# Performance work log

Measured on AMD Instinct MI355X. Metric: run time of the kernel, lower is better.

## Reference

```python
import jax, jax.numpy as jnp
import numpy as np

BS, N, IN_F, OUT_F, HEADS = 32, 512, 256, 128, 4
NEG_SLOPE = 0.2


def setup_inputs() -> dict:
    key = jax.random.key(0)
    k1, k2, k3, k4, k5 = jax.random.split(key, 5)
    inputs = jax.random.normal(k1, (BS, N, IN_F), dtype=jnp.float32)
    adj = (jax.random.uniform(k2, (BS, N, N)) > 0.5).astype(jnp.float32)
    # xavier_normal-style init with relu gain sqrt(2)
    w = jax.random.normal(k3, (IN_F, HEADS * OUT_F), dtype=jnp.float32) * (
        np.sqrt(2.0) * np.sqrt(2.0 / (IN_F + HEADS * OUT_F))
    )
    a_i = jax.random.normal(k4, (HEADS, OUT_F, 1), dtype=jnp.float32) * (
        np.sqrt(2.0) * np.sqrt(2.0 / (OUT_F + 1))
    )
    a_j = jax.random.normal(k5, (HEADS, OUT_F, 1), dtype=jnp.float32) * (
        np.sqrt(2.0) * np.sqrt(2.0 / (OUT_F + 1))
    )
    bias = jnp.zeros((HEADS * OUT_F,), dtype=jnp.float32)
    return {"inputs": inputs, "adj": adj, "w": w, "a_i": a_i, "a_j": a_j, "bias": bias}


def reference(inputs, adj, w, a_i, a_j, bias):
    bs, n, _ = inputs.shape
    H, D = a_i.shape[0], a_i.shape[1]
    # self_loop_type == 2: adjacency unchanged
    # project: [bs, n, H, D]
    h = jnp.matmul(inputs, w).reshape(bs, n, H, D)
    # additive attention coefficients: [bs, n, H]
    coeff_i = jnp.einsum('bnhd,hdo->bnho', h, a_i)[..., 0]
    coeff_j = jnp.einsum('bnhd,hdo->bnho', h, a_j)[..., 0]
    # broadcast-sum scores e[b, i, j, h], leaky relu
    e = jax.nn.leaky_relu(coeff_i[:, :, None, :] + coeff_j[:, None, :, :],
                          negative_slope=NEG_SLOPE)
    adj_h = adj[..., None]  # [bs, n, n, 1], broadcasts over heads
    masked_e = jnp.where(adj_h <= 0, jnp.float32(-1e9), e)
    # softmax over neighbor axis j (dim 2), then re-mask
    attention = jax.nn.softmax(masked_e, axis=2) * adj_h
    # dropout = 0.0 -> no-op; normalize=False, average=False
    # per-head aggregation, all heads at once: out[b,i,h,d] = sum_j att[b,i,j,h] h[b,j,h,d]
    out = jnp.einsum('bijh,bjhd->bihd', attention, h).reshape(bs, n, H * D)
    return out + bias
```

## Files before the change

### kernel.cpp

```cpp
#include <hip/hip_runtime.h>
#include <hip/hip_cooperative_groups.h>

namespace cg = cooperative_groups;

#define BSZ 32
#define NN 512
#define INF 256
#define NH 4
#define HD 512
#define NEG_SLOPE 0.2f

typedef __attribute__((ext_vector_type(8))) short bf16x8;
typedef __attribute__((ext_vector_type(8))) unsigned short ushort8;
typedef __attribute__((ext_vector_type(4))) float f32x4;

static __device__ __forceinline__ unsigned short f2bf(float f) {
    unsigned u = __builtin_bit_cast(unsigned, f);
    return (unsigned short)((u + 0x7FFFu + ((u >> 16) & 1u)) >> 16);
}

static __device__ __forceinline__ bf16x8 pk8(float4 a, float4 b) {
    unsigned d0, d1, d2, d3;
    asm("v_cvt_pk_bf16_f32 %0, %1, %2" : "=v"(d0) : "v"(a.x), "v"(a.y));
    asm("v_cvt_pk_bf16_f32 %0, %1, %2" : "=v"(d1) : "v"(a.z), "v"(a.w));
    asm("v_cvt_pk_bf16_f32 %0, %1, %2" : "=v"(d2) : "v"(b.x), "v"(b.y));
    asm("v_cvt_pk_bf16_f32 %0, %1, %2" : "=v"(d3) : "v"(b.z), "v"(b.w));
    uint4 u; u.x = d0; u.y = d1; u.z = d2; u.w = d3;
    return __builtin_bit_cast(bf16x8, u);
}

static __device__ __forceinline__ void gl_lds16(const void* g, void* l) {
    __builtin_amdgcn_global_load_lds(
        (const __attribute__((address_space(1))) unsigned int*)g,
        (__attribute__((address_space(3))) unsigned int*)l, 16, 0, 0);
}

__global__ __launch_bounds__(256, 4) void mega(
    const float* __restrict__ x, const float* __restrict__ adj,
    const float* __restrict__ w, const float* __restrict__ ai,
    const float* __restrict__ aj, const float* __restrict__ bias,
    float* __restrict__ out, unsigned short* __restrict__ wB,
    unsigned short* __restrict__ hB, float* __restrict__ ciT,
    float* __restrict__ cjT, unsigned char* __restrict__ mbB)
{
    __shared__ __align__(16) char smem[32768];
    const int tid = threadIdx.x;
    const int lane = tid & 63, wave = tid >> 6;
    const int l15 = lane & 15, g = lane >> 4;
    const int bid = blockIdx.x;

    if (bid < 512) {
        int gid = bid * 256 + tid;
        int c = gid & 511, k = gid >> 9;
        int kb = k >> 5, gg = (k >> 3) & 3, e = k & 7;
        wB[(((size_t)(kb * 4 + gg) * 512) + c) * 8 + e] = f2bf(w[(size_t)k * 512 + c]);
    }
    {
        const int row0 = bid * 16 + wave * 4;
        #pragma unroll
        for (int rr = 0; rr < 4; ++rr) {
            const float* ap = adj + (size_t)(row0 + rr) * NN + lane * 8;
            float4 a0 = *(const float4*)ap;
            float4 a1 = *(const float4*)(ap + 4);
            unsigned byte = 0;
            byte |= (a0.x > 0.f) ? 1u   : 0u;
            byte |= (a0.y > 0.f) ? 2u   : 0u;
            byte |= (a0.z > 0.f) ? 4u   : 0u;
            byte |= (a0.w > 0.f) ? 8u   : 0u;
            byte |= (a1.x > 0.f) ? 16u  : 0u;
            byte |= (a1.y > 0.f) ? 32u  : 0u;
            byte |= (a1.z > 0.f) ? 64u  : 0u;
            byte |= (a1.w > 0.f) ? 128u : 0u;
            mbB[(size_t)(row0 + rr) * 64 + lane] = (unsigned char)byte;
        }
    }
    cg::this_grid().sync();

    if (bid < 512) {
        unsigned short* hs = (unsigned short*)smem;
        const int row0 = bid * 32;

        f32x4 acc[2][8] = {};
        const float* xp0 = x + (size_t)(row0 + l15) * INF + g * 8;
        const float* xp1 = xp0 + 16 * INF;
        const unsigned short* bp = wB + ((size_t)g * 512 + (size_t)wave * 128 + l15) * 8;

        #pragma unroll
        for (int kb = 0; kb < 8; ++kb) {
            float4 f0 = *(const float4*)(xp0 + kb * 32);
            float4 f1 = *(const float4*)(xp0 + kb * 32 + 4);
            float4 f2 = *(const float4*)(xp1 + kb * 32);
            float4 f3 = *(const float4*)(xp1 + kb * 32 + 4);
            bf16x8 a0 = pk8(f0, f1);
            bf16x8 a1 = pk8(f2, f3);
            #pragma unroll
            for (int nf = 0; nf < 8; ++nf) {
                bf16x8 bv = *(const bf16x8*)(bp + (size_t)kb * 16384 + nf * 128);
                acc[0][nf] = __builtin_amdgcn_mfma_f32_16x16x32_bf16(a0, bv, acc[0][nf], 0, 0, 0);
                acc[1][nf] = __builtin_amdgcn_mfma_f32_16x16x32_bf16(a1, bv, acc[1][nf], 0, 0, 0);
            }
        }

        float aiv[8], ajv[8];
        #pragma unroll
        for (int nf = 0; nf < 8; ++nf) {
            aiv[nf] = ai[wave * 128 + nf * 16 + l15];
            ajv[nf] = aj[wave * 128 + nf * 16 + l15];
        }
        const int b = row0 >> 9;
        const int nloc0 = row0 & 511;
        const int kb2 = nloc0 >> 5;

        #pragma unroll
        for (int m = 0; m < 2; ++m) {
            float pi[4] = {0,0,0,0}, pj[4] = {0,0,0,0};
            #pragma unroll
            for (int nf = 0; nf < 8; ++nf)
                #pragma unroll
                for (int reg = 0; reg < 4; ++reg) {
                    pi[reg] = fmaf(acc[m][nf][reg], aiv[nf], pi[reg]);
                    pj[reg] = fmaf(acc[m][nf][reg], ajv[nf], pj[reg]);
                }
            #pragma unroll
            for (int reg = 0; reg < 4; ++reg) {
                #pragma unroll
                for (int off = 1; off < 16; off <<= 1) {
                    pi[reg] += __shfl_xor(pi[reg], off);
                    pj[reg] += __shfl_xor(pj[reg], off);
                }
            }
            if (l15 == 0) {
                #pragma unroll
                for (int reg = 0; reg < 4; ++reg) {
                    int n = nloc0 + 16 * m + 4 * g + reg;
                    ciT[((size_t)(wave * BSZ + b) * NN) + n] = pi[reg];
                    cjT[((size_t)(wave * BSZ + b) * NN) + n] = pj[reg];
                }
            }
            #pragma unroll
            for (int reg = 0; reg < 4; ++reg) {
                int jloc = 16 * m + 4 * g + reg;
                int g2 = jloc >> 3, e = jloc & 7;
                #pragma unroll
                for (int nf = 0; nf < 8; ++nf)
                    hs[wave * 4096 + nf * 512 + g2 * 128 + l15 * 8 + e] =
                        f2bf(acc[m][nf][reg]);
            }
        }
        __syncthreads();
        {
            ushort8* dst = (ushort8*)(hB + (((size_t)(b * 4 + wave) * 16 + kb2) * 4096));
            const ushort8* src = (const ushort8*)(hs + wave * 4096);
            #pragma unroll
            for (int it = 0; it < 8; ++it)
                dst[it * 64 + lane] = src[it * 64 + lane];
        }
    }
    cg::this_grid().sync();

    {
        unsigned short (*Bst)[4096] = (unsigned short(*)[4096])smem;
        float* cjh  = (float*)(smem + 16384);
        float* cih  = (float*)(smem + 18432);
        unsigned (*maskS)[17] = (unsigned(*)[17])(smem + 18688);
        float* Mpart = (float*)(smem + 23040);
        const unsigned* mb = (const unsigned*)mbB;

        const int orig = bid;
        const int swz = (orig & 7) * 128 + (orig >> 3);
        const int b  = swz >> 5;
        const int h  = (swz >> 3) & 3;
        const int i0 = (swz & 7) * 64;

        const char* gslab = (const char*)(hB + (size_t)(b * NH + h) * 65536);

        gl_lds16(gslab + wave * 2048 + lane * 16,        (char*)&Bst[0][0] + wave * 2048);
        gl_lds16(gslab + wave * 2048 + 1024 + lane * 16, (char*)&Bst[0][0] + wave * 2048 + 1024);

        {
            const float* src = cjT + (size_t)(h * BSZ + b) * NN;
            float v0 = src[tid], v1 = src[tid + 256];
            cjh[tid] = v0; cjh[tid + 256] = v1;
            float mv = fmaxf(v0, v1);
            #pragma unroll
            for (int off = 32; off; off >>= 1) mv = fmaxf(mv, __shfl_xor(mv, off));
            if (lane == 0) Mpart[wave] = mv;
            if (tid < 64) cih[tid] = ciT[(size_t)(h * BSZ + b) * NN + i0 + tid];
            uint4 m4 = ((const uint4*)(mb + ((size_t)b * NN + i0) * 16))[tid];
            int base = tid * 4, row = base >> 4, wi = base & 15;
            maskS[row][wi] = m4.x; maskS[row][wi + 1] = m4.y;
            maskS[row][wi + 2] = m4.z; maskS[row][wi + 3] = m4.w;
        }
        __syncthreads();

        const float M = fmaxf(fmaxf(Mpart[0], Mpart[1]), fmaxf(Mpart[2], Mpart[3]));
        const float bc = cih[wave * 16 + l15];
        float smx = bc + M;
        const float mrow = fmaxf(smx, NEG_SLOPE * smx);

        float bvv[8];
        #pragma unroll
        for (int nf = 0; nf < 8; ++nf) bvv[nf] = bias[h * 128 + nf * 16 + l15];

        bf16x8 ones;
        #pragma unroll
        for (int e = 0; e < 8; ++e) ones[e] = (short)0x3F80;

        f32x4 acc[8] = {};
        f32x4 accs = {};
        int cur = 0;
        const unsigned* mrowp = maskS[wave * 16 + l15];

        for (int kb = 0; kb < 16; ++kb) {
            if (kb < 15) {
                const char* gs = gslab + (size_t)(kb + 1) * 8192 + wave * 2048 + lane * 16;
                char* ld = (char*)&Bst[cur ^ 1][0] + wave * 2048;
                gl_lds16(gs, ld);
                gl_lds16(gs + 1024, ld + 1024);
            }

            float4 cva = *(const float4*)&cjh[kb * 32 + g * 8];
            float4 cvb = *(const float4*)&cjh[kb * 32 + g * 8 + 4];
            float cj8[8] = {cva.x, cva.y, cva.z, cva.w, cvb.x, cvb.y, cvb.z, cvb.w};
            unsigned byte = (mrowp[kb] >> (g * 8)) & 0xFFu;
            float p[8];
            #pragma unroll
            for (int e = 0; e < 8; ++e) {
                float s = bc + cj8[e];
                s = fmaxf(s, NEG_SLOPE * s);
                float pe = __expf(s - mrow);
                p[e] = ((byte >> e) & 1u) ? pe : 0.f;
            }
            unsigned d0, d1, d2, d3;
            asm("v_cvt_pk_bf16_f32 %0, %1, %2" : "=v"(d0) : "v"(p[0]), "v"(p[1]));
            asm("v_cvt_pk_bf16_f32 %0, %1, %2" : "=v"(d1) : "v"(p[2]), "v"(p[3]));
            asm("v_cvt_pk_bf16_f32 %0, %1, %2" : "=v"(d2) : "v"(p[4]), "v"(p[5]));
            asm("v_cvt_pk_bf16_f32 %0, %1, %2" : "=v"(d3) : "v"(p[6]), "v"(p[7]));
            uint4 u; u.x = d0; u.y = d1; u.z = d2; u.w = d3;
            bf16x8 av = __builtin_bit_cast(bf16x8, u);

            const char* bb = (const char*)&Bst[cur][0] + lane * 16;
            bf16x8 bfr[8];
            #pragma unroll
            for (int nf = 0; nf < 8; ++nf)
                bfr[nf] = *(const bf16x8*)(bb + nf * 1024);

            #pragma unroll
            for (int nf = 0; nf < 8; ++nf)
                acc[nf] = __builtin_amdgcn_mfma_f32_16x16x32_bf16(av, bfr[nf], acc[nf], 0, 0, 0);
            accs = __builtin_amdgcn_mfma_f32_16x16x32_bf16(av, ones, accs, 0, 0, 0);

            if (kb < 15) { __syncthreads(); cur ^= 1; }
        }

        #pragma unroll
        for (int reg = 0; reg < 4; ++reg) {
            float sum = accs[reg];
            float inv = sum > 0.f ? 1.f / sum : 0.f;
            const int i = i0 + wave * 16 + g * 4 + reg;
            #pragma unroll
            for (int nf = 0; nf < 8; ++nf) {
                int colg = h * 128 + nf * 16 + l15;
                out[(size_t)(b * NN + i) * HD + colg] = acc[nf][reg] * inv + bvv[nf];
            }
        }
    }
}

__global__ __launch_bounds__(256) void k_prep(
    const float* __restrict__ w, unsigned short* __restrict__ wB,
    const float* __restrict__ adj, unsigned char* __restrict__ mbB)
{
    const int bid = blockIdx.x;
    if (bid < 2048) {
        const int lane = threadIdx.x & 63, wave = threadIdx.x >> 6;
        const int row0 = bid * 8 + wave * 2;
        #pragma unroll
        for (int rr = 0; rr < 2; ++rr) {
            const float* ap = adj + (size_t)(row0 + rr) * NN + lane * 8;
            float4 a0 = *(const float4*)ap;
            float4 a1 = *(const float4*)(ap + 4);
            unsigned byte = 0;
            byte |= (a0.x > 0.f) ? 1u : 0u;  byte |= (a0.y > 0.f) ? 2u : 0u;
            byte |= (a0.z > 0.f) ? 4u : 0u;  byte |= (a0.w > 0.f) ? 8u : 0u;
            byte |= (a1.x > 0.f) ? 16u : 0u; byte |= (a1.y > 0.f) ? 32u : 0u;
            byte |= (a1.z > 0.f) ? 64u : 0u; byte |= (a1.w > 0.f) ? 128u : 0u;
            mbB[(size_t)(row0 + rr) * 64 + lane] = (unsigned char)byte;
        }
    } else {
        int gid = (bid - 2048) * 256 + threadIdx.x;
        int c = gid & 511, k = gid >> 9;
        int kb = k >> 5, g = (k >> 3) & 3, e = k & 7;
        wB[(((size_t)(kb * 4 + g) * 512) + c) * 8 + e] = f2bf(w[(size_t)k * 512 + c]);
    }
}

__global__ __launch_bounds__(256) void k_proj(
    const float* __restrict__ x, const unsigned short* __restrict__ wB,
    const float* __restrict__ ai, const float* __restrict__ aj,
    unsigned short* __restrict__ hB, float* __restrict__ ciT, float* __restrict__ cjT)
{
    __shared__ unsigned short hs[NH * 4096];
    const int tid = threadIdx.x;
    const int lane = tid & 63, head = tid >> 6;
    const int l15 = lane & 15, g = lane >> 4;
    const int row0 = blockIdx.x * 32;

    f32x4 acc[2][8] = {};
    const float* xp0 = x + (size_t)(row0 + l15) * INF + g * 8;
    const float* xp1 = xp0 + 16 * INF;
    const unsigned short* bp = wB + ((size_t)g * 512 + head * 128 + l15) * 8;

    #pragma unroll
    for (int kb = 0; kb < 8; ++kb) {
        float4 f0 = *(const float4*)(xp0 + kb * 32);
        float4 f1 = *(const float4*)(xp0 + kb * 32 + 4);
        float4 f2 = *(const float4*)(xp1 + kb * 32);
        float4 f3 = *(const float4*)(xp1 + kb * 32 + 4);
        bf16x8 a0 = pk8(f0, f1);
        bf16x8 a1 = pk8(f2, f3);
        #pragma unroll
        for (int nf = 0; nf < 8; ++nf) {
            bf16x8 bv = *(const bf16x8*)(bp + (size_t)kb * 16384 + nf * 128);
            acc[0][nf] = __builtin_amdgcn_mfma_f32_16x16x32_bf16(a0, bv, acc[0][nf], 0, 0, 0);
            acc[1][nf] = __builtin_amdgcn_mfma_f32_16x16x32_bf16(a1, bv, acc[1][nf], 0, 0, 0);
        }
    }

    float aiv[8], ajv[8];
    #pragma unroll
    for (int nf = 0; nf < 8; ++nf) {
        aiv[nf] = ai[head * 128 + nf * 16 + l15];
        ajv[nf] = aj[head * 128 + nf * 16 + l15];
    }
    const int b = row0 >> 9;
    const int nloc0 = row0 & 511;
    const int kb2 = nloc0 >> 5;

    #pragma unroll
    for (int m = 0; m < 2; ++m) {
        float pi[4] = {0,0,0,0}, pj[4] = {0,0,0,0};
        #pragma unroll
        for (int nf = 0; nf < 8; ++nf)
            #pragma unroll
            for (int reg = 0; reg < 4; ++reg) {
                pi[reg] = fmaf(acc[m][nf][reg], aiv[nf], pi[reg]);
                pj[reg] = fmaf(acc[m][nf][reg], ajv[nf], pj[reg]);
            }
        #pragma unroll
        for (int reg = 0; reg < 4; ++reg) {
            #pragma unroll
            for (int off = 1; off < 16; off <<= 1) {
                pi[reg] += __shfl_xor(pi[reg], off);
                pj[reg] += __shfl_xor(pj[reg], off);
            }
        }
        if (l15 == 0) {
            #pragma unroll
            for (int reg = 0; reg < 4; ++reg) {
                int n = nloc0 + 16 * m + 4 * g + reg;
                ciT[((size_t)(head * BSZ + b) * NN) + n] = pi[reg];
                cjT[((size_t)(head * BSZ + b) * NN) + n] = pj[reg];
            }
        }
        #pragma unroll
        for (int reg = 0; reg < 4; ++reg) {
            int jloc = 16 * m + 4 * g + reg;
            int g2 = jloc >> 3, e = jloc & 7;
            #pragma unroll
            for (int nf = 0; nf < 8; ++nf)
                hs[head * 4096 + nf * 512 + g2 * 128 + l15 * 8 + e] =
                    f2bf(acc[m][nf][reg]);
        }
    }
    __syncthreads();
    {
        ushort8* dst = (ushort8*)(hB + (((size_t)(b * 4 + head) * 16 + kb2) * 4096));
        const ushort8* src = (const ushort8*)(hs + head * 4096);
        #pragma unroll
        for (int it = 0; it < 8; ++it)
            dst[it * 64 + lane] = src[it * 64 + lane];
    }
}

__global__ __launch_bounds__(256, 4) void k_attn(
    const unsigned short* __restrict__ hB, const float* __restrict__ ciT,
    const float* __restrict__ cjT, const unsigned* __restrict__ mb,
    const float* __restrict__ bias, float* __restrict__ out)
{
    __shared__ __align__(16) unsigned short Bst[2][4096];
    __shared__ __align__(16) float cjh[NN];
    __shared__ float cih[64];
    __shared__ unsigned maskS[64][17];
    __shared__ float Mpart[4];

    const int tid = threadIdx.x;
    const int lane = tid & 63, wave = tid >> 6;
    const int l15 = lane & 15, g = lane >> 4;

    const int orig = blockIdx.x;
    const int swz = (orig & 7) * 128 + (orig >> 3);
    const int b  = swz >> 5;
    const int h  = (swz >> 3) & 3;
    const int i0 = (swz & 7) * 64;

    const char* gslab = (const char*)(hB + (size_t)(b * NH + h) * 65536);

    gl_lds16(gslab + wave * 2048 + lane * 16,        (char*)&Bst[0][0] + wave * 2048);
    gl_lds16(gslab + wave * 2048 + 1024 + lane * 16, (char*)&Bst[0][0] + wave * 2048 + 1024);

    {
        const float* src = cjT + (size_t)(h * BSZ + b) * NN;
        float v0 = src[tid], v1 = src[tid + 256];
        cjh[tid] = v0; cjh[tid + 256] = v1;
        float mv = fmaxf(v0, v1);
        #pragma unroll
        for (int off = 32; off; off >>= 1) mv = fmaxf(mv, __shfl_xor(mv, off));
        if (lane == 0) Mpart[wave] = mv;
        if (tid < 64) cih[tid] = ciT[(size_t)(h * BSZ + b) * NN + i0 + tid];
        uint4 m4 = ((const uint4*)(mb + ((size_t)b * NN + i0) * 16))[tid];
        int base = tid * 4, row = base >> 4, wi = base & 15;
        maskS[row][wi] = m4.x; maskS[row][wi + 1] = m4.y;
        maskS[row][wi + 2] = m4.z; maskS[row][wi + 3] = m4.w;
    }
    __syncthreads();

    const float M = fmaxf(fmaxf(Mpart[0], Mpart[1]), fmaxf(Mpart[2], Mpart[3]));
    const float bc = cih[wave * 16 + l15];
    float smx = bc + M;
    const float mrow = fmaxf(smx, NEG_SLOPE * smx);

    float bvv[8];
    #pragma unroll
    for (int nf = 0; nf < 8; ++nf) bvv[nf] = bias[h * 128 + nf * 16 + l15];

    bf16x8 ones;
    #pragma unroll
    for (int e = 0; e < 8; ++e) ones[e] = (short)0x3F80;

    f32x4 acc[8] = {};
    f32x4 accs = {};
    int cur = 0;
    const unsigned* mrowp = maskS[wave * 16 + l15];

    for (int kb = 0; kb < 16; ++kb) {
        if (kb < 15) {
            const char* gs = gslab + (size_t)(kb + 1) * 8192 + wave * 2048 + lane * 16;
            char* ld = (char*)&Bst[cur ^ 1][0] + wave * 2048;
            gl_lds16(gs, ld);
            gl_lds16(gs + 1024, ld + 1024);
        }

        float4 cva = *(const float4*)&cjh[kb * 32 + g * 8];
        float4 cvb = *(const float4*)&cjh[kb * 32 + g * 8 + 4];
        float cj8[8] = {cva.x, cva.y, cva.z, cva.w, cvb.x, cvb.y, cvb.z, cvb.w};
        unsigned byte = (mrowp[kb] >> (g * 8)) & 0xFFu;
        float p[8];
        #pragma unroll
        for (int e = 0; e < 8; ++e) {
            float s = bc + cj8[e];
            s = fmaxf(s, NEG_SLOPE * s);
            float pe = __expf(s - mrow);
            p[e] = ((byte >> e) & 1u) ? pe : 0.f;
        }
        unsigned d0, d1, d2, d3;
        asm("v_cvt_pk_bf16_f32 %0, %1, %2" : "=v"(d0) : "v"(p[0]), "v"(p[1]));
        asm("v_cvt_pk_bf16_f32 %0, %1, %2" : "=v"(d1) : "v"(p[2]), "v"(p[3]));
        asm("v_cvt_pk_bf16_f32 %0, %1, %2" : "=v"(d2) : "v"(p[4]), "v"(p[5]));
        asm("v_cvt_pk_bf16_f32 %0, %1, %2" : "=v"(d3) : "v"(p[6]), "v"(p[7]));
        uint4 u; u.x = d0; u.y = d1; u.z = d2; u.w = d3;
        bf16x8 av = __builtin_bit_cast(bf16x8, u);

        const char* bb = (const char*)&Bst[cur][0] + lane * 16;
        bf16x8 bfr[8];
        #pragma unroll
        for (int nf = 0; nf < 8; ++nf)
            bfr[nf] = *(const bf16x8*)(bb + nf * 1024);

        #pragma unroll
        for (int nf = 0; nf < 8; ++nf)
            acc[nf] = __builtin_amdgcn_mfma_f32_16x16x32_bf16(av, bfr[nf], acc[nf], 0, 0, 0);
        accs = __builtin_amdgcn_mfma_f32_16x16x32_bf16(av, ones, accs, 0, 0, 0);

        if (kb < 15) { __syncthreads(); cur ^= 1; }
    }

    #pragma unroll
    for (int reg = 0; reg < 4; ++reg) {
        float sum = accs[reg];
        float inv = sum > 0.f ? 1.f / sum : 0.f;
        const int i = i0 + wave * 16 + g * 4 + reg;
        #pragma unroll
        for (int nf = 0; nf < 8; ++nf) {
            int colg = h * 128 + nf * 16 + l15;
            out[(size_t)(b * NN + i) * HD + colg] = acc[nf][reg] * inv + bvv[nf];
        }
    }
}

extern "C" void kernel_launch(void* const* d_in, const int* in_sizes, int n_in,
                              void* d_out, int out_size, void* d_ws, size_t ws_size,
                              hipStream_t stream)
{
    const float* x    = (const float*)d_in[0];
    const float* adj  = (const float*)d_in[1];
    const float* w    = (const float*)d_in[2];
    const float* ai   = (const float*)d_in[3];
    const float* aj   = (const float*)d_in[4];
    const float* bias = (const float*)d_in[5];
    float* out = (float*)d_out;

    char* ws = (char*)d_ws;
    unsigned short* wB = (unsigned short*)ws;
    unsigned short* hB = (unsigned short*)(ws + 262144);
    float* ciT         = (float*)(ws + 17039360);
    float* cjT         = (float*)(ws + 17301504);
    unsigned char* mbB = (unsigned char*)(ws + 17563648);

    int maxB = 0;
    hipError_t e = hipOccupancyMaxActiveBlocksPerMultiprocessor(
        &maxB, (const void*)mega, 256, 0);
    if (e == hipSuccess && maxB >= 4) {
        void* args[] = {(void*)&x, (void*)&adj, (void*)&w, (void*)&ai, (void*)&aj,
                        (void*)&bias, (void*)&out, (void*)&wB, (void*)&hB,
                        (void*)&ciT, (void*)&cjT, (void*)&mbB};
        hipLaunchCooperativeKernel((const void*)mega, dim3(1024), dim3(256),
                                   args, 0, stream);
    } else {
        k_prep<<<2560, 256, 0, stream>>>(w, wB, adj, mbB);
        k_proj<<<BSZ * NN / 32, 256, 0, stream>>>(x, wB, ai, aj, hB, ciT, cjT);
        k_attn<<<BSZ * NH * (NN / 64), 256, 0, stream>>>(hB, ciT, cjT,
                                                         (const unsigned*)mbB, bias, out);
    }
}
```

Baseline: 49.93 us.

## Replace grid-wide syncs with per-batch atomic flag dependencies

Swaps the two cooperative grid barriers for finer-grained atomic counters. Half the blocks convert the weights and build the adjacency bitmask while the other half wait only for the weight conversion before projecting. Attention blocks for a batch then wait only on that batch's 32 producers. The aim is to overlap the phases and avoid full-grid stalls, at the cost of a memset launch and spin-wait polling. Correctness relies on all blocks being co-resident.

```diff
diff --git a/kernel.cpp b/kernel.cpp
--- a/kernel.cpp
+++ b/kernel.cpp
@@ -1,7 +1,4 @@
 #include <hip/hip_runtime.h>
-#include <hip/hip_cooperative_groups.h>
-
-namespace cg = cooperative_groups;
 
 #define BSZ 32
 #define NN 512
@@ -35,55 +32,78 @@
         (__attribute__((address_space(3))) unsigned int*)l, 16, 0, 0);
 }
 
-__global__ __launch_bounds__(256, 4) void mega(
+__global__ __launch_bounds__(256, 4) void mega2(
     const float* __restrict__ x, const float* __restrict__ adj,
     const float* __restrict__ w, const float* __restrict__ ai,
     const float* __restrict__ aj, const float* __restrict__ bias,
     float* __restrict__ out, unsigned short* __restrict__ wB,
     unsigned short* __restrict__ hB, float* __restrict__ ciT,
-    float* __restrict__ cjT, unsigned char* __restrict__ mbB)
+    float* __restrict__ cjT, unsigned char* __restrict__ mbB,
+    unsigned* __restrict__ flags)
 {
     __shared__ __align__(16) char smem[32768];
     const int tid = threadIdx.x;
     const int lane = tid & 63, wave = tid >> 6;
     const int l15 = lane & 15, g = lane >> 4;
-    const int bid = blockIdx.x;
-
-    if (bid < 512) {
-        int gid = bid * 256 + tid;
-        int c = gid & 511, k = gid >> 9;
-        int kb = k >> 5, gg = (k >> 3) & 3, e = k & 7;
-        wB[(((size_t)(kb * 4 + gg) * 512) + c) * 8 + e] = f2bf(w[(size_t)k * 512 + c]);
-    }
-    {
-        const int row0 = bid * 16 + wave * 4;
-        #pragma unroll
-        for (int rr = 0; rr < 4; ++rr) {
-            const float* ap = adj + (size_t)(row0 + rr) * NN + lane * 8;
-            float4 a0 = *(const float4*)ap;
-            float4 a1 = *(const float4*)(ap + 4);
-            unsigned byte = 0;
-            byte |= (a0.x > 0.f) ? 1u   : 0u;
-            byte |= (a0.y > 0.f) ? 2u   : 0u;
-            byte |= (a0.z > 0.f) ? 4u   : 0u;
-            byte |= (a0.w > 0.f) ? 8u   : 0u;
-            byte |= (a1.x > 0.f) ? 16u  : 0u;
-            byte |= (a1.y > 0.f) ? 32u  : 0u;
-            byte |= (a1.z > 0.f) ? 64u  : 0u;
-            byte |= (a1.w > 0.f) ? 128u : 0u;
-            mbB[(size_t)(row0 + rr) * 64 + lane] = (unsigned char)byte;
-        }
-    }
-    cg::this_grid().sync();
-
-    if (bid < 512) {
+
+    const int orig = blockIdx.x;
+    const int swz = (orig & 7) * 128 + (orig >> 3);
+    const int b   = swz >> 5;
+    const int sub = swz & 31;
+
+    if (sub >= 16) {
+        {
+            int s = b * 16 + (sub - 16);
+            int gid = s * 256 + tid;
+            int c = gid & 511, k = gid >> 9;
+            int kb = k >> 5, gg = (k >> 3) & 3, e = k & 7;
+            wB[(((size_t)(kb * 4 + gg) * 512) + c) * 8 + e] =
+                f2bf(w[(size_t)k * 512 + c]);
+        }
+        __syncthreads();
+        __threadfence();
+        if (tid == 0)
+            __hip_atomic_fetch_add(&flags[32], 1u, __ATOMIC_RELEASE,
+                                   __HIP_MEMORY_SCOPE_AGENT);
+        {
+            const int r0 = b * NN + (sub - 16) * 32 + wave * 8;
+            #pragma unroll
+            for (int rr = 0; rr < 8; ++rr) {
+                const float* ap = adj + (size_t)(r0 + rr) * NN + lane * 8;
+                float4 a0 = *(const float4*)ap;
+                float4 a1 = *(const float4*)(ap + 4);
+                unsigned byte = 0;
+                byte |= (a0.x > 0.f) ? 1u : 0u;  byte |= (a0.y > 0.f) ? 2u : 0u;
+                byte |= (a0.z > 0.f) ? 4u : 0u;  byte |= (a0.w > 0.f) ? 8u : 0u;
+                byte |= (a1.x > 0.f) ? 16u : 0u; byte |= (a1.y > 0.f) ? 32u : 0u;
+                byte |= (a1.z > 0.f) ? 64u : 0u; byte |= (a1.w > 0.f) ? 128u : 0u;
+                mbB[(size_t)(r0 + rr) * 64 + lane] = (unsigned char)byte;
+            }
+        }
+        __syncthreads();
+        __threadfence();
+        if (tid == 0)
+            __hip_atomic_fetch_add(&flags[b], 1u, __ATOMIC_RELEASE,
+                                   __HIP_MEMORY_SCOPE_AGENT);
+    } else {
+        if (tid == 0) {
+            while (__hip_atomic_load(&flags[32], __ATOMIC_ACQUIRE,
+                                     __HIP_MEMORY_SCOPE_AGENT) < 512u)
+                __builtin_amdgcn_s_sleep(2);
+        }
+        __syncthreads();
+        __threadfence();
+
         unsigned short* hs = (unsigned short*)smem;
-        const int row0 = bid * 32;
+        const int head = wave;
+        const int nloc0 = sub * 32;
+        const int row0 = b * NN + nloc0;
+        const int kb2 = sub;
 
         f32x4 acc[2][8] = {};
         const float* xp0 = x + (size_t)(row0 + l15) * INF + g * 8;
         const float* xp1 = xp0 + 16 * INF;
-        const unsigned short* bp = wB + ((size_t)g * 512 + (size_t)wave * 128 + l15) * 8;
+        const unsigned short* bp = wB + ((size_t)g * 512 + head * 128 + l15) * 8;
 
         #pragma unroll
         for (int kb = 0; kb < 8; ++kb) {
@@ -104,12 +124,9 @@
         float aiv[8], ajv[8];
         #pragma unroll
         for (int nf = 0; nf < 8; ++nf) {
-            aiv[nf] = ai[wave * 128 + nf * 16 + l15];
-            ajv[nf] = aj[wave * 128 + nf * 16 + l15];
-        }
-        const int b = row0 >> 9;
-        const int nloc0 = row0 & 511;
-        const int kb2 = nloc0 >> 5;
+            aiv[nf] = ai[head * 128 + nf * 16 + l15];
+            ajv[nf] = aj[head * 128 + nf * 16 + l15];
+        }
 
         #pragma unroll
         for (int m = 0; m < 2; ++m) {
@@ -133,8 +150,8 @@
                 #pragma unroll
                 for (int reg = 0; reg < 4; ++reg) {
                     int n = nloc0 + 16 * m + 4 * g + reg;
-                    ciT[((size_t)(wave * BSZ + b) * NN) + n] = pi[reg];
-                    cjT[((size_t)(wave * BSZ + b) * NN) + n] = pj[reg];
+                    ciT[((size_t)(head * BSZ + b) * NN) + n] = pi[reg];
+                    cjT[((size_t)(head * BSZ + b) * NN) + n] = pj[reg];
                 }
             }
             #pragma unroll
@@ -143,20 +160,32 @@
                 int g2 = jloc >> 3, e = jloc & 7;
                 #pragma unroll
                 for (int nf = 0; nf < 8; ++nf)
-                    hs[wave * 4096 + nf * 512 + g2 * 128 + l15 * 8 + e] =
+                    hs[head * 4096 + nf * 512 + g2 * 128 + l15 * 8 + e] =
                         f2bf(acc[m][nf][reg]);
             }
         }
         __syncthreads();
         {
-            ushort8* dst = (ushort8*)(hB + (((size_t)(b * 4 + wave) * 16 + kb2) * 4096));
-            const ushort8* src = (const ushort8*)(hs + wave * 4096);
+            ushort8* dst = (ushort8*)(hB + (((size_t)(b * 4 + head) * 16 + kb2) * 4096));
+            const ushort8* src = (const ushort8*)(hs + head * 4096);
             #pragma unroll
             for (int it = 0; it < 8; ++it)
                 dst[it * 64 + lane] = src[it * 64 + lane];
         }
-    }
-    cg::this_grid().sync();
+        __syncthreads();
+        __threadfence();
+        if (tid == 0)
+            __hip_atomic_fetch_add(&flags[b], 1u, __ATOMIC_RELEASE,
+                                   __HIP_MEMORY_SCOPE_AGENT);
+    }
+
+    if (tid == 0) {
+        while (__hip_atomic_load(&flags[b], __ATOMIC_ACQUIRE,
+                                 __HIP_MEMORY_SCOPE_AGENT) < 32u)
+            __builtin_amdgcn_s_sleep(2);
+    }
+    __syncthreads();
+    __threadfence();
 
     {
         unsigned short (*Bst)[4096] = (unsigned short(*)[4096])smem;
@@ -166,9 +195,6 @@
         float* Mpart = (float*)(smem + 23040);
         const unsigned* mb = (const unsigned*)mbB;
 
-        const int orig = bid;
-        const int swz = (orig & 7) * 128 + (orig >> 3);
-        const int b  = swz >> 5;
         const int h  = (swz >> 3) & 3;
         const int i0 = (swz & 7) * 64;
 
@@ -516,15 +542,18 @@
     float* ciT         = (float*)(ws + 17039360);
     float* cjT         = (float*)(ws + 17301504);
     unsigned char* mbB = (unsigned char*)(ws + 17563648);
+    unsigned* flags    = (unsigned*)(ws + 18612224);
+
+    hipMemsetAsync(flags, 0, 256, stream);
 
     int maxB = 0;
     hipError_t e = hipOccupancyMaxActiveBlocksPerMultiprocessor(
-        &maxB, (const void*)mega, 256, 0);
+        &maxB, (const void*)mega2, 256, 0);
     if (e == hipSuccess && maxB >= 4) {
         void* args[] = {(void*)&x, (void*)&adj, (void*)&w, (void*)&ai, (void*)&aj,
                         (void*)&bias, (void*)&out, (void*)&wB, (void*)&hB,
-                        (void*)&ciT, (void*)&cjT, (void*)&mbB};
-        hipLaunchCooperativeKernel((const void*)mega, dim3(1024), dim3(256),
+                        (void*)&ciT, (void*)&cjT, (void*)&mbB, (void*)&flags};
+        hipLaunchCooperativeKernel((const void*)mega2, dim3(1024), dim3(256),
                                    args, 0, stream);
     } else {
         k_prep<<<2560, 256, 0, stream>>>(w, wB, adj, mbB);
```

New measurement: 54.89 us. 1.1x slower.
